# Performance work log

Measured on AMD Instinct MI355X. Metric: run time of the kernel, lower is better.

The kernel has to match this reference:

```python
import jax, jax.numpy as jnp
import numpy as np

B, S, E, H = 2, 2048, 1024, 16
D = E // H  # head_dim = 64


def setup_inputs() -> dict:
    key = jax.random.key(0)
    ks = jax.random.split(key, 6)
    scale = 1.0 / np.sqrt(E)
    return {
        "x": jax.random.normal(ks[0], (B, S, E), dtype=jnp.float32),
        "Wqkv_w": jax.random.normal(ks[1], (3 * E, E), dtype=jnp.float32) * scale,
        "Wqkv_b": jax.random.normal(ks[2], (3 * E,), dtype=jnp.float32) * 0.01,
        "out_w": jax.random.normal(ks[3], (E, E), dtype=jnp.float32) * scale,
        "out_b": jax.random.normal(ks[4], (E,), dtype=jnp.float32) * 0.01,
        "distance_decay": jax.random.normal(ks[5], (1,), dtype=jnp.float32),
    }


def reference(x, Wqkv_w, Wqkv_b, out_w, out_b, distance_decay):
    b, s, e = x.shape
    # fused QKV projection: (b, s, 3e) -> three (b, h, s, d)
    qkv = x @ Wqkv_w.T + Wqkv_b
    qkv = qkv.reshape(b, s, 3, H, D).transpose(2, 0, 3, 1, 4)  # (3, b, h, s, d)
    q, k, v = qkv[0], qkv[1], qkv[2]
    # scores scaled by 1/sqrt(head_dim)
    scores = jnp.einsum("bhsd,bhtd->bhst", q, k) / jnp.sqrt(jnp.asarray(D, x.dtype))
    # multiplicative exponential distance decay: exp(-|a| * |i-j|)
    idx = jnp.arange(s, dtype=x.dtype)
    dist = jnp.abs(idx[:, None] - idx[None, :])  # (s, s)
    decay = jnp.exp(-jnp.abs(distance_decay[0]) * dist)
    scores = scores * decay  # broadcast over (b, h)
    attn = jax.nn.softmax(scores, axis=-1)
    out = jnp.einsum("bhst,bhtd->bhsd", attn, v)  # (b, h, s, d)
    out = out.transpose(0, 2, 1, 3).reshape(b, s, e)  # (b, s, e)
    return out @ out_w.T + out_b
```

## Files before the change

### kernel.cpp

```cpp
#include <hip/hip_runtime.h>
#include <hip/hip_bf16.h>

#define BN 2
#define SDIM 2048
#define EDIM 1024
#define HN 16
#define DDIM 64

typedef __attribute__((ext_vector_type(8))) short bfrag;
typedef __attribute__((ext_vector_type(4))) float ffrag;

__device__ __forceinline__ ffrag mfma16(bfrag a, bfrag b, ffrag c) {
    return __builtin_amdgcn_mfma_f32_16x16x32_bf16(a, b, c, 0, 0, 0);
}

__device__ __forceinline__ ushort f2bf(float f) {
    union { float f; unsigned u; } un;
    un.f = f;
    unsigned u = un.u;
    u += 0x7fffu + ((u >> 16) & 1u);
    return (ushort)(u >> 16);
}

__device__ __forceinline__ uint pkbf2(float a, float b) {
    __hip_bfloat162 h = __float22bfloat162_rn(make_float2(a, b));
    union { __hip_bfloat162 h; uint u; } cv;
    cv.h = h;
    return cv.u;
}

__device__ __forceinline__ void gld16(const void* g, void* l) {
    __builtin_amdgcn_global_load_lds((const __attribute__((address_space(1))) void*)g,
                                     (__attribute__((address_space(3))) void*)l,
                                     16, 0, 0);
}

__global__ __launch_bounds__(256) void to_bf16_3(const float* __restrict__ a, ushort* __restrict__ oa, int na,
                                                 const float* __restrict__ b, ushort* __restrict__ ob, int nb,
                                                 const float* __restrict__ c, ushort* __restrict__ oc, int nc) {
    int i = (blockIdx.x * 256 + threadIdx.x) * 4;
    const float* src;
    ushort* dst;
    if (i < na)                { src = a + i;            dst = oa + i; }
    else if (i < na + nb)      { src = b + (i - na);     dst = ob + (i - na); }
    else if (i < na + nb + nc) { src = c + (i - na - nb); dst = oc + (i - na - nb); }
    else return;
    float4 v = *(const float4*)src;
    uint2 u;
    u.x = pkbf2(v.x, v.y);
    u.y = pkbf2(v.z, v.w);
    *(uint2*)dst = u;
}

template <int UNUSED>
__global__ __launch_bounds__(512, 2) void gemm256_qkv(const ushort* __restrict__ A,
                                                      const ushort* __restrict__ Bt,
                                                      const float* __restrict__ bias,
                                                      ushort* __restrict__ Cout,
                                                      float* __restrict__ T,
                                                      int M, int N, int K) {
    constexpr int BM = 256, BNT = 192;
    constexpr int A_USH = BM * 64;
    constexpr int B_USH = BNT * 64;
    constexpr int BUF_USH = A_USH + B_USH;
    __shared__ ushort lds[2 * BUF_USH];
    __shared__ float Tred[4 * BNT];

    const int tid  = threadIdx.x;
    const int wave = tid >> 6;
    const int lane = tid & 63;
    const int ln16 = lane & 15;
    const int quad = lane >> 4;
    const int wm   = wave >> 2;
    const int wn   = wave & 3;
    const int bm   = blockIdx.x * BM;
    const int bn   = blockIdx.y * BNT;

    const int r0 = tid >> 3;
    const int c0 = ((tid & 7) - r0) & 7;
    const ushort* Abase = A  + (size_t)(bm + r0) * K + c0 * 8;
    const ushort* Bbase = Bt + (size_t)(bn + r0) * K + c0 * 8;
    const int ldst0 = wave * 512;

    const int Ra = wm * 128 + ln16;
    const int Rb = wn * 48 + ln16;
    int aoff[2], boff[2];
#pragma unroll
    for (int kb = 0; kb < 2; ++kb) {
        aoff[kb] = Ra * 64 + ((kb * 4 + quad + Ra) & 7) * 8;
        boff[kb] = A_USH + Rb * 64 + ((kb * 4 + quad + Rb) & 7) * 8;
    }

    ffrag acc[8][3];
#pragma unroll
    for (int mi = 0; mi < 8; ++mi)
#pragma unroll
        for (int ni = 0; ni < 3; ++ni)
            acc[mi][ni] = (ffrag){0.f, 0.f, 0.f, 0.f};

    const int nt = K >> 6;

    auto stA = [&](int buf, int t, int rnd) {
        gld16(Abase + (size_t)rnd * 64 * K + t * 64,
              &lds[buf * BUF_USH + rnd * 4096 + ldst0]);
    };
    auto stB = [&](int buf, int t, int rnd) {
        gld16(Bbase + (size_t)rnd * 64 * K + t * 64,
              &lds[buf * BUF_USH + A_USH + rnd * 4096 + ldst0]);
    };

    stA(0, 0, 0); stA(0, 0, 1); stA(0, 0, 2); stA(0, 0, 3);
    stB(0, 0, 0); stB(0, 0, 1); stB(0, 0, 2);
    stA(1, 1, 0); stA(1, 1, 2);
    stB(1, 1, 0); stB(1, 1, 1); stB(1, 1, 2);
    asm volatile("s_waitcnt vmcnt(5)" ::: "memory");
    __builtin_amdgcn_s_barrier();

    for (int t = 0; t < nt; ++t) {
        const int buf = t & 1;
        const ushort* Al = &lds[buf * BUF_USH];
        const bool h1 = (t + 1) < nt;
        const bool h2 = (t + 2) < nt;
        bfrag bfr[3][2];
#pragma unroll
        for (int p = 0; p < 4; ++p) {
            bfrag afr[2][2];
#pragma unroll
            for (int m2 = 0; m2 < 2; ++m2)
#pragma unroll
                for (int kb = 0; kb < 2; ++kb)
                    afr[m2][kb] = *(const bfrag*)(Al + aoff[kb] + (p * 2 + m2) * 1024);
            if (p == 0) {
#pragma unroll
                for (int ni = 0; ni < 3; ++ni)
#pragma unroll
                    for (int kb = 0; kb < 2; ++kb)
                        bfr[ni][kb] = *(const bfrag*)(Al + boff[kb] + ni * 1024);
            }
            if (p == 0 && h1) stA(buf ^ 1, t + 1, 1);
            if (p == 1 && h1) stA(buf ^ 1, t + 1, 3);
            if (p == 2 && h2) { stA(buf, t + 2, 0); stA(buf, t + 2, 2); stB(buf, t + 2, 0); }
            if (p == 3 && h2) { stB(buf, t + 2, 1); stB(buf, t + 2, 2); }

            __builtin_amdgcn_s_barrier();
            asm volatile("s_waitcnt lgkmcnt(0)" ::: "memory");
            __builtin_amdgcn_sched_barrier(0);
            __builtin_amdgcn_s_setprio(1);
#pragma unroll
            for (int m2 = 0; m2 < 2; ++m2)
#pragma unroll
                for (int ni = 0; ni < 3; ++ni)
#pragma unroll
                    for (int kb = 0; kb < 2; ++kb)
                        acc[p * 2 + m2][ni] = mfma16(afr[m2][kb], bfr[ni][kb], acc[p * 2 + m2][ni]);
            __builtin_amdgcn_s_setprio(0);
            if (p == 3) {
                if (h2)      { asm volatile("s_waitcnt vmcnt(5)" ::: "memory"); }
                else if (h1) { asm volatile("s_waitcnt vmcnt(0)" ::: "memory"); }
            }
            __builtin_amdgcn_s_barrier();
        }
    }

    const bool hasV = (bn + BNT - 1) >= 2 * EDIM;
    if (hasV) {
        for (int idx = tid; idx < 4 * BNT; idx += 512) Tred[idx] = 0.f;
        __syncthreads();
    }

#pragma unroll
    for (int mi = 0; mi < 8; ++mi) {
#pragma unroll
        for (int ni = 0; ni < 3; ++ni) {
            int col = bn + wn * 48 + ni * 16 + ln16;
            float bc = bias[col];
            int row0 = bm + wm * 128 + mi * 16 + quad * 4;
            int which = col >> 10;
            int rem = col & 1023;
            int h = rem >> 6;
            int d = rem & 63;
            int b = row0 >> 11;
            int s0 = row0 & 2047;
            if (which == 2) {
                float v0 = acc[mi][ni][0] + bc, v1 = acc[mi][ni][1] + bc;
                float v2 = acc[mi][ni][2] + bc, v3 = acc[mi][ni][3] + bc;
                uint2 pk;
                pk.x = pkbf2(v0, v1);
                pk.y = pkbf2(v2, v3);
                size_t dst = 2ull * (BN * HN * SDIM * DDIM) +
                             (((size_t)(b * HN + h)) * DDIM + d) * SDIM + s0;
                *(uint2*)(Cout + dst) = pk;
                int tl = (wm * 128 + mi * 16 + quad * 4) >> 6;
                int cl = wn * 48 + ni * 16 + ln16;
                atomicAdd(&Tred[tl * BNT + cl], v0 + v1 + v2 + v3);
            } else {
                float sc = (which == 0) ? 0.125f : 1.f;
#pragma unroll
                for (int reg = 0; reg < 4; ++reg) {
                    float v = (acc[mi][ni][reg] + bc) * sc;
                    size_t dst = (size_t)which * (BN * HN * SDIM * DDIM) +
                                 (((size_t)(b * HN + h)) * SDIM + s0 + reg) * DDIM + d;
                    Cout[dst] = f2bf(v);
                }
            }
        }
    }

    if (hasV) {
        __syncthreads();
        for (int idx = tid; idx < 4 * BNT; idx += 512) {
            int tl = idx / BNT, cl = idx % BNT;
            int col = bn + cl;
            if (col >= 2 * EDIM) {
                int rem = col - 2 * EDIM;
                int h = rem >> 6, d = rem & 63;
                int b = bm >> 11;
                int tile_g = ((bm & 2047) >> 6) + tl;
                T[(((size_t)(b * HN + h)) * 32 + tile_g) * 64 + d] = Tred[idx];
            }
        }
    }
}

__global__ __launch_bounds__(512, 4) void gemm128_op(const ushort* __restrict__ A,
                                                     const ushort* __restrict__ Bt,
                                                     const float* __restrict__ bias,
                                                     float* __restrict__ C,
                                                     int M, int N, int K) {
    constexpr int BM = 128, BNT = 128;
    constexpr int A_USH = BM * 64;
    constexpr int B_USH = BNT * 64;
    constexpr int BUF_USH = A_USH + B_USH;
    __shared__ ushort lds[2 * BUF_USH];

    const int tid  = threadIdx.x;
    const int wave = tid >> 6;
    const int lane = tid & 63;
    const int ln16 = lane & 15;
    const int quad = lane >> 4;
    const int wm   = wave >> 2;
    const int wn   = wave & 3;
    const int bm   = blockIdx.x * BM;
    const int bn   = blockIdx.y * BNT;

    const int r0 = tid >> 3;
    const int c0 = ((tid & 7) - r0) & 7;
    const ushort* Abase = A  + (size_t)(bm + r0) * K + c0 * 8;
    const ushort* Bbase = Bt + (size_t)(bn + r0) * K + c0 * 8;
    const int ldst0 = wave * 512;

    const int Ra = wm * 64 + ln16;
    const int Rb = wn * 32 + ln16;
    int aoff[2], boff[2];
#pragma unroll
    for (int kb = 0; kb < 2; ++kb) {
        aoff[kb] = Ra * 64 + ((kb * 4 + quad + Ra) & 7) * 8;
        boff[kb] = A_USH + Rb * 64 + ((kb * 4 + quad + Rb) & 7) * 8;
    }

    ffrag acc[4][2];
#pragma unroll
    for (int mi = 0; mi < 4; ++mi)
#pragma unroll
        for (int ni = 0; ni < 2; ++ni)
            acc[mi][ni] = (ffrag){0.f, 0.f, 0.f, 0.f};

    const int nt = K >> 6;

    auto stA = [&](int buf, int t, int rnd) {
        gld16(Abase + (size_t)rnd * 64 * K + t * 64,
              &lds[buf * BUF_USH + rnd * 4096 + ldst0]);
    };
    auto stB = [&](int buf, int t, int rnd) {
        gld16(Bbase + (size_t)rnd * 64 * K + t * 64,
              &lds[buf * BUF_USH + A_USH + rnd * 4096 + ldst0]);
    };

    stA(0, 0, 0); stA(0, 0, 1); stB(0, 0, 0); stB(0, 0, 1);
    stA(1, 1, 0); stA(1, 1, 1); stB(1, 1, 0); stB(1, 1, 1);
    asm volatile("s_waitcnt vmcnt(4)" ::: "memory");
    __builtin_amdgcn_s_barrier();

    for (int t = 0; t < nt; ++t) {
        const int buf = t & 1;
        const ushort* Al = &lds[buf * BUF_USH];
        bfrag afr[4][2], bfr[2][2];
#pragma unroll
        for (int mi = 0; mi < 4; ++mi)
#pragma unroll
            for (int kb = 0; kb < 2; ++kb)
                afr[mi][kb] = *(const bfrag*)(Al + aoff[kb] + mi * 1024);
#pragma unroll
        for (int ni = 0; ni < 2; ++ni)
#pragma unroll
            for (int kb = 0; kb < 2; ++kb)
                bfr[ni][kb] = *(const bfrag*)(Al + boff[kb] + ni * 1024);
        asm volatile("s_waitcnt lgkmcnt(0)" ::: "memory");
        __builtin_amdgcn_sched_barrier(0);
        __builtin_amdgcn_s_barrier();

        if (t + 2 < nt) {
            stA(buf, t + 2, 0); stA(buf, t + 2, 1);
            stB(buf, t + 2, 0); stB(buf, t + 2, 1);
        }

        __builtin_amdgcn_s_setprio(1);
#pragma unroll
        for (int mi = 0; mi < 4; ++mi)
#pragma unroll
            for (int ni = 0; ni < 2; ++ni)
#pragma unroll
                for (int kb = 0; kb < 2; ++kb)
                    acc[mi][ni] = mfma16(afr[mi][kb], bfr[ni][kb], acc[mi][ni]);
        __builtin_amdgcn_s_setprio(0);

        if (t + 2 < nt)      { asm volatile("s_waitcnt vmcnt(4)" ::: "memory"); }
        else if (t + 1 < nt) { asm volatile("s_waitcnt vmcnt(0)" ::: "memory"); }
        __builtin_amdgcn_s_barrier();
    }

#pragma unroll
    for (int mi = 0; mi < 4; ++mi) {
#pragma unroll
        for (int ni = 0; ni < 2; ++ni) {
            int col = bn + wn * 32 + ni * 16 + ln16;
            float bc = bias[col];
            int row0 = bm + wm * 64 + mi * 16 + quad * 4;
#pragma unroll
            for (int reg = 0; reg < 4; ++reg)
                C[(size_t)(row0 + reg) * N + col] = acc[mi][ni][reg] + bc;
        }
    }
}

__global__ __launch_bounds__(512, 4) void flash_attn(const ushort* __restrict__ Qb,
                                                     const ushort* __restrict__ Kb,
                                                     const ushort* __restrict__ Vtb,
                                                     const float* __restrict__ decay_ptr,
                                                     const float* __restrict__ T,
                                                     ushort* __restrict__ Ob) {
    __shared__ ushort KVs[2][2][4096];
    __shared__ ushort Pb[128][72];
    __shared__ float  Fv[64];

    const int tid  = threadIdx.x;
    const int wave = tid >> 6;
    const int lane = tid & 63;
    const int ln16 = lane & 15;
    const int quad = lane >> 4;

    const int bh = blockIdx.y;
    const int q0 = blockIdx.x * 128;
    const size_t head_off = (size_t)bh * SDIM * DDIM;
    const float absa = fabsf(decay_ptr[0]);
    const float LOG2E = 1.442695041f;
    const float M0L2 = -17.3123404f;
    const float E12 = 6.144212353e-6f;

    int Dstar = (absa > 1e-5f) ? (int)ceilf(16.0f / absa) : (4 * SDIM);
    int lo = q0 - 63 - Dstar; if (lo < 0) lo = 0;
    int hi = q0 + 127 + Dstar; if (hi > SDIM - 1) hi = SDIM - 1;
    const int tlo = lo >> 6;
    const int thi = hi >> 6;
    const int ntiles = thi - tlo + 1;

    if (tid < 64) {
        const float* Tp = T + (size_t)bh * 32 * 64;
        float s = 0.f;
        for (int k = 0; k < tlo; ++k)      s += Tp[k * 64 + tid];
        for (int k = thi + 1; k < 32; ++k) s += Tp[k * 64 + tid];
        Fv[tid] = s;
    }

    auto stageKV = [&](int t0, int buf) {
        int g0 = wave * 64;
        int g  = g0 + lane;
        int r  = g >> 3;
        int c  = (g - r) & 7;
        gld16(Kb  + head_off + (size_t)(t0 + r) * DDIM + c * 8,
              (ushort*)&KVs[buf][0][0] + g0 * 8);
        gld16(Vtb + head_off + (size_t)r * SDIM + t0 + c * 8,
              (ushort*)&KVs[buf][1][0] + g0 * 8);
    };

#pragma unroll
    for (int p = 0; p < 2; ++p) {
        int idx = p * 512 + tid;
        int r = idx >> 3, c = (idx & 7) * 8;
        *(uint4*)&Pb[r][c] = *(const uint4*)(Qb + head_off + (size_t)(q0 + r) * DDIM + c);
    }
    stageKV(tlo * 64, 0);
    __syncthreads();

    bfrag aq[2];
#pragma unroll
    for (int kb = 0; kb < 2; ++kb)
        aq[kb] = *(const bfrag*)&Pb[wave * 16 + ln16][kb * 32 + quad * 8];

    bfrag ones;
#pragma unroll
    for (int i = 0; i < 8; ++i) ones[i] = (short)0x3F80;

    float EcB[4], FcB[4], Epw[4], Fpw[4];
#pragma unroll
    for (int reg = 0; reg < 4; ++reg) {
        int cr = quad * 4 + reg;
        EcB[reg] = __expf(-absa * (float)(15 - cr));
        FcB[reg] = __expf(-absa * (float)cr);
    }
#pragma unroll
    for (int ni = 0; ni < 4; ++ni) {
        Epw[ni] = __expf(-absa * (float)(16 * (3 - ni)));
        Fpw[ni] = __expf(-absa * (float)(16 * ni));
    }
    const float Er = __expf(-absa * (float)ln16);
    const float Fr = __expf(-absa * (float)(15 - ln16));

    ffrag lacc = (ffrag){0.f, 0.f, 0.f, 0.f};
    ffrag o[4];
#pragma unroll
    for (int ni = 0; ni < 4; ++ni) o[ni] = (ffrag){0.f, 0.f, 0.f, 0.f};

    const int m = wave * 16 + ln16;

    for (int it = 0; it < ntiles; ++it) {
        const int t0 = (tlo + it) * 64;
        const int buf = it & 1;
        if (it + 1 < ntiles) stageKV(t0 + 64, buf ^ 1);

        const ushort* Kt = &KVs[buf][0][0];
        const ushort* Vt = &KVs[buf][1][0];

        ffrag sc[4];
#pragma unroll
        for (int ni = 0; ni < 4; ++ni) {
            ffrag a = (ffrag){0.f, 0.f, 0.f, 0.f};
            const int rk = ni * 16 + ln16;
#pragma unroll
            for (int kb = 0; kb < 2; ++kb) {
                bfrag kf = *(const bfrag*)&Kt[rk * 64 + ((kb * 4 + quad + rk) & 7) * 8];
                a = mfma16(kf, aq[kb], a);
            }
            sc[ni] = a;
        }

        const int ds = q0 + wave * 16 - t0;
        float hh = 0.f;
        if (ds >= 64)       hh = __expf(-absa * (float)(ds - 63)) * Er * LOG2E;
        else if (ds <= -16) hh = __expf(-absa * (float)(-ds - 15)) * Fr * LOG2E;

#pragma unroll
        for (int ni = 0; ni < 4; ++ni) {
            float f0, f1, f2, f3;
            if (ds >= 64) {
                float hn = hh * Epw[ni];
                f0 = hn * EcB[0]; f1 = hn * EcB[1]; f2 = hn * EcB[2]; f3 = hn * EcB[3];
            } else if (ds <= -16) {
                float hn = hh * Fpw[ni];
                f0 = hn * FcB[0]; f1 = hn * FcB[1]; f2 = hn * FcB[2]; f3 = hn * FcB[3];
            } else {
                int c0 = ni * 16 + quad * 4;
                f0 = __expf(-absa * fabsf((float)(ds + ln16 - c0)))     * LOG2E;
                f1 = __expf(-absa * fabsf((float)(ds + ln16 - c0 - 1))) * LOG2E;
                f2 = __expf(-absa * fabsf((float)(ds + ln16 - c0 - 2))) * LOG2E;
                f3 = __expf(-absa * fabsf((float)(ds + ln16 - c0 - 3))) * LOG2E;
            }
            float p0 = exp2f(fmaf(sc[ni][0], f0, M0L2));
            float p1 = exp2f(fmaf(sc[ni][1], f1, M0L2));
            float p2 = exp2f(fmaf(sc[ni][2], f2, M0L2));
            float p3 = exp2f(fmaf(sc[ni][3], f3, M0L2));
            uint2 pk;
            pk.x = pkbf2(p0, p1);
            pk.y = pkbf2(p2, p3);
            *(uint2*)&Pb[m][ni * 16 + quad * 4] = pk;
        }

        bfrag ap[2];
#pragma unroll
        for (int kb = 0; kb < 2; ++kb)
            ap[kb] = *(const bfrag*)&Pb[m][kb * 32 + quad * 8];

#pragma unroll
        for (int kb = 0; kb < 2; ++kb)
            lacc = mfma16(ones, ap[kb], lacc);
#pragma unroll
        for (int ni = 0; ni < 4; ++ni) {
            const int rv = ni * 16 + ln16;
#pragma unroll
            for (int kb = 0; kb < 2; ++kb) {
                bfrag vf = *(const bfrag*)&Vt[rv * 64 + ((kb * 4 + quad + rv) & 7) * 8];
                o[ni] = mfma16(vf, ap[kb], o[ni]);
            }
        }
        __syncthreads();
    }

    const float farl = E12 * (float)(SDIM - 64 * ntiles);
    const float inv = 1.f / (lacc[0] + farl);
    const int b = bh / HN, h = bh % HN;
    const int s = q0 + m;
    ushort* dst = Ob + ((size_t)(b * SDIM + s)) * EDIM + h * DDIM + quad * 4;
#pragma unroll
    for (int ni = 0; ni < 4; ++ni) {
        int d0 = ni * 16 + quad * 4;
        float v0 = (o[ni][0] + E12 * Fv[d0 + 0]) * inv;
        float v1 = (o[ni][1] + E12 * Fv[d0 + 1]) * inv;
        float v2 = (o[ni][2] + E12 * Fv[d0 + 2]) * inv;
        float v3 = (o[ni][3] + E12 * Fv[d0 + 3]) * inv;
        uint2 pk;
        pk.x = pkbf2(v0, v1);
        pk.y = pkbf2(v2, v3);
        *(uint2*)(dst + ni * 16) = pk;
    }
}

extern "C" void kernel_launch(void* const* d_in, const int* in_sizes, int n_in,
                              void* d_out, int out_size, void* d_ws, size_t ws_size,
                              hipStream_t stream) {
    const float* x      = (const float*)d_in[0];
    const float* Wqkv_w = (const float*)d_in[1];
    const float* Wqkv_b = (const float*)d_in[2];
    const float* out_w  = (const float*)d_in[3];
    const float* out_b  = (const float*)d_in[4];
    const float* dd     = (const float*)d_in[5];

    char* ws = (char*)d_ws;
    const size_t MB = 1024 * 1024;
    ushort* xb    = (ushort*)(ws + 0 * MB);
    ushort* wqkvb = (ushort*)(ws + 8 * MB);
    ushort* owb   = (ushort*)(ws + 14 * MB);
    ushort* qkvb  = (ushort*)(ws + 16 * MB);
    ushort* ob    = (ushort*)(ws + 40 * MB);
    float*  Tp    = (float*)(ws + 48 * MB);

    const int n_x = BN * SDIM * EDIM;
    const int n_w = 3 * EDIM * EDIM;
    const int n_o = EDIM * EDIM;
    const int HSD = BN * HN * SDIM * DDIM;

    to_bf16_3<<<(n_x + n_w + n_o) / 1024, 256, 0, stream>>>(
        x, xb, n_x, Wqkv_w, wqkvb, n_w, out_w, owb, n_o);

    gemm256_qkv<0><<<dim3(16, 16), 512, 0, stream>>>(xb, wqkvb, Wqkv_b, qkvb, Tp,
                                                     BN * SDIM, 3 * EDIM, EDIM);

    flash_attn<<<dim3(SDIM / 128, BN * HN), 512, 0, stream>>>(
        qkvb, qkvb + HSD, qkvb + 2 * HSD, dd, Tp, ob);

    gemm128_op<<<dim3(32, 8), 512, 0, stream>>>(ob, owb, out_b, (float*)d_out,
                                                BN * SDIM, EDIM, EDIM);
}
```

Baseline: 172.6 us.

## Shrink QKV GEMM tile to 128x192 with XCD-aware block remap and shuffle V-sum

```diff
diff --git a/kernel.cpp b/kernel.cpp
--- a/kernel.cpp
+++ b/kernel.cpp
@@ -53,18 +53,17 @@
 }
 
 template <int UNUSED>
-__global__ __launch_bounds__(512, 2) void gemm256_qkv(const ushort* __restrict__ A,
+__global__ __launch_bounds__(512, 4) void gemm192_qkv(const ushort* __restrict__ A,
                                                       const ushort* __restrict__ Bt,
                                                       const float* __restrict__ bias,
                                                       ushort* __restrict__ Cout,
                                                       float* __restrict__ T,
                                                       int M, int N, int K) {
-    constexpr int BM = 256, BNT = 192;
+    constexpr int BM = 128, BNT = 192;
     constexpr int A_USH = BM * 64;
     constexpr int B_USH = BNT * 64;
     constexpr int BUF_USH = A_USH + B_USH;
     __shared__ ushort lds[2 * BUF_USH];
-    __shared__ float Tred[4 * BNT];
 
     const int tid  = threadIdx.x;
     const int wave = tid >> 6;
@@ -73,8 +72,14 @@
     const int quad = lane >> 4;
     const int wm   = wave >> 2;
     const int wn   = wave & 3;
-    const int bm   = blockIdx.x * BM;
-    const int bn   = blockIdx.y * BNT;
+
+    const int lid  = blockIdx.y * 32 + blockIdx.x;
+    const int xcd  = lid & 7;
+    const int rank = lid >> 3;
+    const int tx   = (xcd & 3) * 8 + (rank & 7);
+    const int ty   = (xcd >> 2) * 8 + (rank >> 3);
+    const int bm   = tx * BM;
+    const int bn   = ty * BNT;
 
     const int r0 = tid >> 3;
     const int c0 = ((tid & 7) - r0) & 7;
@@ -82,7 +87,7 @@
     const ushort* Bbase = Bt + (size_t)(bn + r0) * K + c0 * 8;
     const int ldst0 = wave * 512;
 
-    const int Ra = wm * 128 + ln16;
+    const int Ra = wm * 64 + ln16;
     const int Rb = wn * 48 + ln16;
     int aoff[2], boff[2];
 #pragma unroll
@@ -91,9 +96,9 @@
         boff[kb] = A_USH + Rb * 64 + ((kb * 4 + quad + Rb) & 7) * 8;
     }
 
-    ffrag acc[8][3];
-#pragma unroll
-    for (int mi = 0; mi < 8; ++mi)
+    ffrag acc[4][3];
+#pragma unroll
+    for (int mi = 0; mi < 4; ++mi)
 #pragma unroll
         for (int ni = 0; ni < 3; ++ni)
             acc[mi][ni] = (ffrag){0.f, 0.f, 0.f, 0.f};
@@ -109,11 +114,10 @@
               &lds[buf * BUF_USH + A_USH + rnd * 4096 + ldst0]);
     };
 
-    stA(0, 0, 0); stA(0, 0, 1); stA(0, 0, 2); stA(0, 0, 3);
+    stA(0, 0, 0); stA(0, 0, 1);
     stB(0, 0, 0); stB(0, 0, 1); stB(0, 0, 2);
-    stA(1, 1, 0); stA(1, 1, 2);
     stB(1, 1, 0); stB(1, 1, 1); stB(1, 1, 2);
-    asm volatile("s_waitcnt vmcnt(5)" ::: "memory");
+    asm volatile("s_waitcnt vmcnt(3)" ::: "memory");
     __builtin_amdgcn_s_barrier();
 
     for (int t = 0; t < nt; ++t) {
@@ -124,12 +128,10 @@
         bfrag bfr[3][2];
 #pragma unroll
         for (int p = 0; p < 4; ++p) {
-            bfrag afr[2][2];
-#pragma unroll
-            for (int m2 = 0; m2 < 2; ++m2)
-#pragma unroll
-                for (int kb = 0; kb < 2; ++kb)
-                    afr[m2][kb] = *(const bfrag*)(Al + aoff[kb] + (p * 2 + m2) * 1024);
+            bfrag afr[2];
+#pragma unroll
+            for (int kb = 0; kb < 2; ++kb)
+                afr[kb] = *(const bfrag*)(Al + aoff[kb] + p * 1024);
             if (p == 0) {
 #pragma unroll
                 for (int ni = 0; ni < 3; ++ni)
@@ -137,44 +139,37 @@
                     for (int kb = 0; kb < 2; ++kb)
                         bfr[ni][kb] = *(const bfrag*)(Al + boff[kb] + ni * 1024);
             }
-            if (p == 0 && h1) stA(buf ^ 1, t + 1, 1);
-            if (p == 1 && h1) stA(buf ^ 1, t + 1, 3);
-            if (p == 2 && h2) { stA(buf, t + 2, 0); stA(buf, t + 2, 2); stB(buf, t + 2, 0); }
-            if (p == 3 && h2) { stB(buf, t + 2, 1); stB(buf, t + 2, 2); }
+            if (p == 0 && h1) stA(buf ^ 1, t + 1, 0);
+            if (p == 1 && h1) stA(buf ^ 1, t + 1, 1);
+            if (p == 1 && h2) stB(buf, t + 2, 0);
+            if (p == 2 && h2) stB(buf, t + 2, 1);
+            if (p == 3 && h2) stB(buf, t + 2, 2);
 
             __builtin_amdgcn_s_barrier();
             asm volatile("s_waitcnt lgkmcnt(0)" ::: "memory");
             __builtin_amdgcn_sched_barrier(0);
             __builtin_amdgcn_s_setprio(1);
 #pragma unroll
-            for (int m2 = 0; m2 < 2; ++m2)
-#pragma unroll
-                for (int ni = 0; ni < 3; ++ni)
-#pragma unroll
-                    for (int kb = 0; kb < 2; ++kb)
-                        acc[p * 2 + m2][ni] = mfma16(afr[m2][kb], bfr[ni][kb], acc[p * 2 + m2][ni]);
+            for (int ni = 0; ni < 3; ++ni)
+#pragma unroll
+                for (int kb = 0; kb < 2; ++kb)
+                    acc[p][ni] = mfma16(afr[kb], bfr[ni][kb], acc[p][ni]);
             __builtin_amdgcn_s_setprio(0);
             if (p == 3) {
-                if (h2)      { asm volatile("s_waitcnt vmcnt(5)" ::: "memory"); }
+                if (h2)      { asm volatile("s_waitcnt vmcnt(3)" ::: "memory"); }
                 else if (h1) { asm volatile("s_waitcnt vmcnt(0)" ::: "memory"); }
             }
             __builtin_amdgcn_s_barrier();
         }
     }
 
-    const bool hasV = (bn + BNT - 1) >= 2 * EDIM;
-    if (hasV) {
-        for (int idx = tid; idx < 4 * BNT; idx += 512) Tred[idx] = 0.f;
-        __syncthreads();
-    }
-
-#pragma unroll
-    for (int mi = 0; mi < 8; ++mi) {
+#pragma unroll
+    for (int mi = 0; mi < 4; ++mi) {
 #pragma unroll
         for (int ni = 0; ni < 3; ++ni) {
             int col = bn + wn * 48 + ni * 16 + ln16;
             float bc = bias[col];
-            int row0 = bm + wm * 128 + mi * 16 + quad * 4;
+            int row0 = bm + wm * 64 + mi * 16 + quad * 4;
             int which = col >> 10;
             int rem = col & 1023;
             int h = rem >> 6;
@@ -190,9 +185,6 @@
                 size_t dst = 2ull * (BN * HN * SDIM * DDIM) +
                              (((size_t)(b * HN + h)) * DDIM + d) * SDIM + s0;
                 *(uint2*)(Cout + dst) = pk;
-                int tl = (wm * 128 + mi * 16 + quad * 4) >> 6;
-                int cl = wn * 48 + ni * 16 + ln16;
-                atomicAdd(&Tred[tl * BNT + cl], v0 + v1 + v2 + v3);
             } else {
                 float sc = (which == 0) ? 0.125f : 1.f;
 #pragma unroll
@@ -206,17 +198,25 @@
         }
     }
 
-    if (hasV) {
-        __syncthreads();
-        for (int idx = tid; idx < 4 * BNT; idx += 512) {
-            int tl = idx / BNT, cl = idx % BNT;
-            int col = bn + cl;
-            if (col >= 2 * EDIM) {
-                int rem = col - 2 * EDIM;
+#pragma unroll
+    for (int ni = 0; ni < 3; ++ni) {
+        int col = bn + wn * 48 + ni * 16 + ln16;
+        if ((col >> 10) == 2) {
+            float s = 0.f;
+#pragma unroll
+            for (int mi = 0; mi < 4; ++mi)
+#pragma unroll
+                for (int reg = 0; reg < 4; ++reg)
+                    s += acc[mi][ni][reg];
+            s += __shfl_xor(s, 16);
+            s += __shfl_xor(s, 32);
+            if (quad == 0) {
+                float bc = bias[col];
+                int rem = col & 1023;
                 int h = rem >> 6, d = rem & 63;
                 int b = bm >> 11;
-                int tile_g = ((bm & 2047) >> 6) + tl;
-                T[(((size_t)(b * HN + h)) * 32 + tile_g) * 64 + d] = Tred[idx];
+                int tile_g = ((bm & 2047) >> 6) + wm;
+                T[(((size_t)(b * HN + h)) * 32 + tile_g) * 64 + d] = s + 64.f * bc;
             }
         }
     }
@@ -541,7 +541,7 @@
     to_bf16_3<<<(n_x + n_w + n_o) / 1024, 256, 0, stream>>>(
         x, xb, n_x, Wqkv_w, wqkvb, n_w, out_w, owb, n_o);
 
-    gemm256_qkv<0><<<dim3(16, 16), 512, 0, stream>>>(xb, wqkvb, Wqkv_b, qkvb, Tp,
+    gemm192_qkv<0><<<dim3(32, 16), 512, 0, stream>>>(xb, wqkvb, Wqkv_b, qkvb, Tp,
                                                      BN * SDIM, 3 * EDIM, EDIM);
 
     flash_attn<<<dim3(SDIM / 128, BN * HN), 512, 0, stream>>>(
```

Measured after the change: 157.8 us. 8.6% less time.
